# Kernel optimization log

Measured on AMD Instinct MI355X. Metric: run time of the kernel, lower is better.

## Reference

```python
import jax, jax.numpy as jnp
import numpy as np

NODE_DIM = 256
HALF = NODE_DIM // 2  # 128

# COCO-17 hierarchical grouping (from the torch module, num_joints == 17)
ORDER_1_HEAD = np.array([0, 1, 2, 3, 4])                                   # group 0: 5 joints
ORDER_1_PAIRS = np.array([(5, 6), (7, 9), (8, 10), (11, 12), (13, 15), (14, 16)])  # groups 1..6
ORDER_2_PAIRS = np.array([(0, 1), (1, 2), (1, 3), (1, 4), (4, 5), (4, 6)])


def setup_inputs() -> dict:
    key = jax.random.key(0)
    ks = jax.random.split(key, 9)
    N = 50000
    s = 0.02
    update = jax.random.normal(ks[0], (N, 17, NODE_DIM), dtype=jnp.float32)
    # first_layer[0]: Linear(node_dim*5 -> node_dim//2)
    W1_0 = jax.random.normal(ks[1], (HALF, 5 * NODE_DIM), dtype=jnp.float32) * s
    b1_0 = jax.random.normal(ks[2], (HALF,), dtype=jnp.float32) * s
    W1 = jax.random.normal(ks[3], (6, HALF, 2 * NODE_DIM), dtype=jnp.float32) * s
    b1 = jax.random.normal(ks[4], (6, HALF), dtype=jnp.float32) * s
    W2 = jax.random.normal(ks[5], (6, HALF, 2 * HALF), dtype=jnp.float32) * s
    b2 = jax.random.normal(ks[6], (6, HALF), dtype=jnp.float32) * s
    # final: Linear(6*HALF -> node_dim)
    Wf = jax.random.normal(ks[7], (NODE_DIM, 6 * HALF), dtype=jnp.float32) * s
    bf = jax.random.normal(ks[8], (NODE_DIM,), dtype=jnp.float32) * s
    return {"update": update, "W1_0": W1_0, "b1_0": b1_0, "W1": W1, "b1": b1,
            "W2": W2, "b2": b2, "Wf": Wf, "bf": bf}


def reference(update, W1_0, b1_0, W1, b1, W2, b2, Wf, bf):
    N = update.shape[0]
    # ---- first layer ----
    # group 0: joints (0..4) concatenated -> [N, 5*D]
    x0 = update[:, ORDER_1_HEAD].reshape(N, -1)
    h0 = jax.nn.relu(x0 @ W1_0.T + b1_0)                       # [N, HALF]
    # groups 1..6: pair gathers -> [N, 6, 2*D], batched small GEMM
    xp = update[:, ORDER_1_PAIRS].reshape(N, 6, -1)            # [N, 6, 2D]
    hp = jax.nn.relu(jnp.einsum('ngd,gkd->ngk', xp, W1) + b1)  # [N, 6, HALF]
    out_1 = jnp.concatenate([h0[:, None], hp], axis=1)         # [N, 7, HALF]
    # ---- second layer: pair gathers over out_1 ----
    x2 = out_1[:, ORDER_2_PAIRS].reshape(N, 6, -1)             # [N, 6, 2*HALF]
    out_2 = jax.nn.relu(jnp.einsum('ngd,gkd->ngk', x2, W2) + b2)  # [N, 6, HALF]
    # ---- final ----
    return jax.nn.relu(out_2.reshape(N, -1) @ Wf.T + bf)       # [N, NODE_DIM]
```

## Files before the change

### kernel.cpp

```cpp
#include <hip/hip_runtime.h>
#include <cstdint>

#define NODE_DIM 256
#define HALF 128
#define NJ 17

typedef __bf16 bf16x8 __attribute__((ext_vector_type(8)));
typedef float f32x4 __attribute__((ext_vector_type(4)));

__device__ __forceinline__ unsigned short f2bf(float f) {
  unsigned int u = __builtin_bit_cast(unsigned int, f);
  u = (u + 0x7FFFu + ((u >> 16) & 1u)) >> 16;
  return (unsigned short)u;
}

__device__ __forceinline__ unsigned int pack2(float lo, float hi) {
  return (unsigned int)f2bf(lo) | ((unsigned int)f2bf(hi) << 16);
}

__device__ const int d_P0[6] = {5, 7, 8, 11, 13, 14};
__device__ const int d_P1[6] = {6, 9, 10, 12, 15, 16};
__device__ const int d_Q0[6] = {0, 1, 1, 1, 4, 4};
__device__ const int d_Q1[6] = {1, 2, 3, 4, 5, 6};

__global__ __launch_bounds__(256) void kconv(
    const float* __restrict__ a, const float* __restrict__ b,
    const float* __restrict__ c, const float* __restrict__ d,
    unsigned short* __restrict__ dst) {
  const int na = 163840, nb = 393216, nc = 196608, nd = 196608;
  const int total = na + nb + nc + nd;
  int i = (blockIdx.x * 256 + threadIdx.x) * 4;
  if (i >= total) return;
  const float* src;
  int off;
  if (i < na) { src = a; off = i; }
  else if (i < na + nb) { src = b; off = i - na; }
  else if (i < na + nb + nc) { src = c; off = i - na - nb; }
  else { src = d; off = i - na - nb - nc; }
  float4 v = *(const float4*)(src + off);
  uint2 p;
  p.x = pack2(v.x, v.y);
  p.y = pack2(v.z, v.w);
  *(uint2*)(dst + i) = p;
}

__global__ __launch_bounds__(256) void k1_layer1(
    const float* __restrict__ upd,
    const unsigned short* __restrict__ w10,
    const unsigned short* __restrict__ w1,
    const float* __restrict__ b10,
    const float* __restrict__ b1,
    unsigned short* __restrict__ out1,
    int N, int ntiles) {
  __shared__ unsigned short sA[64 * 72];
  __shared__ unsigned short sW[128 * 72];

  const int tile = blockIdx.x % ntiles;
  const int g = blockIdx.x / ntiles;
  const int t = threadIdx.x;
  const int lane = t & 63;
  const int wv = t >> 6;
  const int l16 = lane & 15;
  const int quad = lane >> 4;
  const int node0 = tile * 64;

  const int K = (g == 0) ? 1280 : 512;
  const unsigned short* W = (g == 0) ? w10 : (w1 + (size_t)(g - 1) * 128 * 512);

  const int ar = t >> 2, al = t & 3;
  const int wr = t >> 1, wh = t & 1;

  f32x4 acc[8];
#pragma unroll
  for (int i = 0; i < 8; ++i) acc[i] = (f32x4){0.f, 0.f, 0.f, 0.f};

  int n = node0 + ar;
  if (n >= N) n = N - 1;

  const int nchunks = K >> 6;
  for (int kc = 0; kc < nchunks; ++kc) {
    const int kabs = kc << 6;
    int j;
    if (g == 0) j = kabs >> 8;
    else j = (kabs < 256) ? d_P0[g - 1] : d_P1[g - 1];

    const float* src = upd + ((size_t)n * NJ + j) * NODE_DIM + (kabs & 255) + al * 16;
    float4 f0 = *(const float4*)(src + 0);
    float4 f1 = *(const float4*)(src + 4);
    float4 f2 = *(const float4*)(src + 8);
    float4 f3 = *(const float4*)(src + 12);
    const uint4* wsrc = (const uint4*)(W + (size_t)wr * K + kabs + wh * 32);
    uint4 q0 = wsrc[0], q1 = wsrc[1], q2 = wsrc[2], q3 = wsrc[3];

    __syncthreads();
    uint4 pa0, pa1;
    pa0.x = pack2(f0.x, f0.y); pa0.y = pack2(f0.z, f0.w);
    pa0.z = pack2(f1.x, f1.y); pa0.w = pack2(f1.z, f1.w);
    pa1.x = pack2(f2.x, f2.y); pa1.y = pack2(f2.z, f2.w);
    pa1.z = pack2(f3.x, f3.y); pa1.w = pack2(f3.z, f3.w);
    *(uint4*)(sA + ar * 72 + al * 16) = pa0;
    *(uint4*)(sA + ar * 72 + al * 16 + 8) = pa1;
    uint4* dW = (uint4*)(sW + wr * 72 + wh * 32);
    dW[0] = q0; dW[1] = q1; dW[2] = q2; dW[3] = q3;
    __syncthreads();

#pragma unroll
    for (int kk = 0; kk < 64; kk += 32) {
      bf16x8 a = *(const bf16x8*)(sA + (wv * 16 + l16) * 72 + kk + quad * 8);
#pragma unroll
      for (int nt = 0; nt < 8; ++nt) {
        bf16x8 b = *(const bf16x8*)(sW + (nt * 16 + l16) * 72 + kk + quad * 8);
        acc[nt] = __builtin_amdgcn_mfma_f32_16x16x32_bf16(a, b, acc[nt], 0, 0, 0);
      }
    }
  }

  const float* bias = (g == 0) ? b10 : (b1 + (g - 1) * HALF);
#pragma unroll
  for (int nt = 0; nt < 8; ++nt) {
    const float bv = bias[nt * 16 + l16];
#pragma unroll
    for (int r = 0; r < 4; ++r) {
      const int node = node0 + wv * 16 + quad * 4 + r;
      if (node < N) {
        float v = acc[nt][r] + bv;
        v = v > 0.f ? v : 0.f;
        out1[(size_t)node * 896 + g * 128 + nt * 16 + l16] = f2bf(v);
      }
    }
  }
}

__global__ __launch_bounds__(256) void k2_layer2(
    const unsigned short* __restrict__ out1,
    const unsigned short* __restrict__ w2,
    const float* __restrict__ b2,
    unsigned short* __restrict__ out2,
    int N, int ntiles) {
  __shared__ unsigned short sA[64 * 72];
  __shared__ unsigned short sW[128 * 72];

  const int tile = blockIdx.x % ntiles;
  const int g = blockIdx.x / ntiles;
  const int t = threadIdx.x;
  const int lane = t & 63;
  const int wv = t >> 6;
  const int l16 = lane & 15;
  const int quad = lane >> 4;
  const int node0 = tile * 64;

  const unsigned short* W = w2 + (size_t)g * 128 * 256;
  const int ar = t >> 2, al = t & 3;
  const int wr = t >> 1, wh = t & 1;

  f32x4 acc[8];
#pragma unroll
  for (int i = 0; i < 8; ++i) acc[i] = (f32x4){0.f, 0.f, 0.f, 0.f};

  int n = node0 + ar;
  if (n >= N) n = N - 1;
  const int p0 = d_Q0[g], p1 = d_Q1[g];

  for (int kc = 0; kc < 4; ++kc) {
    const int kabs = kc << 6;
    const int grp = (kabs < 128) ? p0 : p1;
    const unsigned short* srcA = out1 + (size_t)n * 896 + grp * 128 + (kabs & 127) + al * 16;
    const uint4* asrc = (const uint4*)srcA;
    uint4 va0 = asrc[0], va1 = asrc[1];
    const uint4* wsrc = (const uint4*)(W + (size_t)wr * 256 + kabs + wh * 32);
    uint4 q0 = wsrc[0], q1 = wsrc[1], q2 = wsrc[2], q3 = wsrc[3];

    __syncthreads();
    uint4* dA = (uint4*)(sA + ar * 72 + al * 16);
    dA[0] = va0; dA[1] = va1;
    uint4* dW = (uint4*)(sW + wr * 72 + wh * 32);
    dW[0] = q0; dW[1] = q1; dW[2] = q2; dW[3] = q3;
    __syncthreads();

#pragma unroll
    for (int kk = 0; kk < 64; kk += 32) {
      bf16x8 a = *(const bf16x8*)(sA + (wv * 16 + l16) * 72 + kk + quad * 8);
#pragma unroll
      for (int nt = 0; nt < 8; ++nt) {
        bf16x8 b = *(const bf16x8*)(sW + (nt * 16 + l16) * 72 + kk + quad * 8);
        acc[nt] = __builtin_amdgcn_mfma_f32_16x16x32_bf16(a, b, acc[nt], 0, 0, 0);
      }
    }
  }

  const float* bias = b2 + g * HALF;
#pragma unroll
  for (int nt = 0; nt < 8; ++nt) {
    const float bv = bias[nt * 16 + l16];
#pragma unroll
    for (int r = 0; r < 4; ++r) {
      const int node = node0 + wv * 16 + quad * 4 + r;
      if (node < N) {
        float v = acc[nt][r] + bv;
        v = v > 0.f ? v : 0.f;
        out2[(size_t)node * 768 + g * 128 + nt * 16 + l16] = f2bf(v);
      }
    }
  }
}

__global__ __launch_bounds__(256) void k3_final(
    const unsigned short* __restrict__ out2,
    const unsigned short* __restrict__ wf,
    const float* __restrict__ bf_,
    float* __restrict__ out,
    int N) {
  __shared__ unsigned short sA[64 * 72];
  __shared__ unsigned short sW[256 * 72];

  const int t = threadIdx.x;
  const int lane = t & 63;
  const int wv = t >> 6;
  const int l16 = lane & 15;
  const int quad = lane >> 4;
  const int node0 = blockIdx.x * 64;

  const int ar = t >> 2, al = t & 3;

  f32x4 acc[16];
#pragma unroll
  for (int i = 0; i < 16; ++i) acc[i] = (f32x4){0.f, 0.f, 0.f, 0.f};

  int n = node0 + ar;
  if (n >= N) n = N - 1;

  for (int kc = 0; kc < 12; ++kc) {
    const int kabs = kc << 6;
    const uint4* asrc = (const uint4*)(out2 + (size_t)n * 768 + kabs + al * 16);
    uint4 va0 = asrc[0], va1 = asrc[1];
    const uint4* wsrc = (const uint4*)(wf + (size_t)t * 768 + kabs);
    uint4 q0 = wsrc[0], q1 = wsrc[1], q2 = wsrc[2], q3 = wsrc[3];
    uint4 q4 = wsrc[4], q5 = wsrc[5], q6 = wsrc[6], q7 = wsrc[7];

    __syncthreads();
    uint4* dA = (uint4*)(sA + ar * 72 + al * 16);
    dA[0] = va0; dA[1] = va1;
    uint4* dW = (uint4*)(sW + t * 72);
    dW[0] = q0; dW[1] = q1; dW[2] = q2; dW[3] = q3;
    dW[4] = q4; dW[5] = q5; dW[6] = q6; dW[7] = q7;
    __syncthreads();

#pragma unroll
    for (int kk = 0; kk < 64; kk += 32) {
      bf16x8 a = *(const bf16x8*)(sA + (wv * 16 + l16) * 72 + kk + quad * 8);
#pragma unroll
      for (int nt = 0; nt < 16; ++nt) {
        bf16x8 b = *(const bf16x8*)(sW + (nt * 16 + l16) * 72 + kk + quad * 8);
        acc[nt] = __builtin_amdgcn_mfma_f32_16x16x32_bf16(a, b, acc[nt], 0, 0, 0);
      }
    }
  }

#pragma unroll
  for (int nt = 0; nt < 16; ++nt) {
    const float bv = bf_[nt * 16 + l16];
#pragma unroll
    for (int r = 0; r < 4; ++r) {
      const int node = node0 + wv * 16 + quad * 4 + r;
      if (node < N) {
        float v = acc[nt][r] + bv;
        v = v > 0.f ? v : 0.f;
        out[(size_t)node * 256 + nt * 16 + l16] = v;
      }
    }
  }
}

extern "C" void kernel_launch(void* const* d_in, const int* in_sizes, int n_in,
                              void* d_out, int out_size, void* d_ws, size_t ws_size,
                              hipStream_t stream) {
  const float* upd = (const float*)d_in[0];
  const float* W10f = (const float*)d_in[1];
  const float* b10 = (const float*)d_in[2];
  const float* W1f = (const float*)d_in[3];
  const float* b1 = (const float*)d_in[4];
  const float* W2f = (const float*)d_in[5];
  const float* b2 = (const float*)d_in[6];
  const float* Wff = (const float*)d_in[7];
  const float* bff = (const float*)d_in[8];

  const int N = in_sizes[0] / (NJ * NODE_DIM);
  const int ntiles = (N + 63) / 64;

  unsigned short* wbf = (unsigned short*)d_ws;
  unsigned short* w10 = wbf;
  unsigned short* w1 = wbf + 163840;
  unsigned short* w2 = wbf + 163840 + 393216;
  unsigned short* wf = wbf + 163840 + 393216 + 196608;
  unsigned short* out1 = (unsigned short*)((char*)d_ws + (size_t)(2u << 20));
  unsigned short* out2 = out1 + (size_t)N * 896;

  kconv<<<(237568 + 255) / 256, 256, 0, stream>>>(W10f, W1f, W2f, Wff, wbf);
  k1_layer1<<<ntiles * 7, 256, 0, stream>>>(upd, w10, w1, b10, b1, out1, N, ntiles);
  k2_layer2<<<ntiles * 6, 256, 0, stream>>>(out1, w2, b2, out2, N, ntiles);
  k3_final<<<ntiles, 256, 0, stream>>>(out2, wf, bff, (float*)d_out, N);
}
```

Before: 1.338 ms.

## Double-buffer GEMM kernels with direct global-to-LDS loads and swizzled LDS

Restructures all three GEMM kernels to double-buffer the shared-memory tiles. Weight and activation tiles are loaded straight into LDS with global_load_lds into an XOR-swizzled layout, so the next K chunk streams in while the current one feeds the MFMAs. Layers 1 and 2 now loop over all groups inside one block per node tile instead of one block per (tile, group). Their outputs are staged through LDS so each node row is written with coalesced 16-byte stores. This removes a barrier per chunk and the register round trip for loads, at the cost of more LDS per block, lower occupancy, and far fewer blocks for layers 1 and 2.

```diff
diff --git a/kernel.cpp b/kernel.cpp
--- a/kernel.cpp
+++ b/kernel.cpp
@@ -16,6 +16,12 @@
 
 __device__ __forceinline__ unsigned int pack2(float lo, float hi) {
   return (unsigned int)f2bf(lo) | ((unsigned int)f2bf(hi) << 16);
+}
+
+__device__ __forceinline__ void gload16(const void* g, void* l) {
+  __builtin_amdgcn_global_load_lds(
+      (const __attribute__((address_space(1))) unsigned int*)g,
+      (__attribute__((address_space(3))) unsigned int*)l, 16, 0, 0);
 }
 
 __device__ const int d_P0[6] = {5, 7, 8, 11, 13, 14};
@@ -44,6 +50,7 @@
   *(uint2*)(dst + i) = p;
 }
 
+
 __global__ __launch_bounds__(256) void k1_layer1(
     const float* __restrict__ upd,
     const unsigned short* __restrict__ w10,
@@ -51,81 +58,121 @@
     const float* __restrict__ b10,
     const float* __restrict__ b1,
     unsigned short* __restrict__ out1,
-    int N, int ntiles) {
-  __shared__ unsigned short sA[64 * 72];
-  __shared__ unsigned short sW[128 * 72];
-
-  const int tile = blockIdx.x % ntiles;
-  const int g = blockIdx.x / ntiles;
+    int N) {
+  __shared__ unsigned short sA[2][64 * 64];
+  __shared__ unsigned short sW[2][128 * 64];
+
   const int t = threadIdx.x;
   const int lane = t & 63;
   const int wv = t >> 6;
   const int l16 = lane & 15;
   const int quad = lane >> 4;
-  const int node0 = tile * 64;
-
-  const int K = (g == 0) ? 1280 : 512;
-  const unsigned short* W = (g == 0) ? w10 : (w1 + (size_t)(g - 1) * 128 * 512);
+  const int node0 = blockIdx.x * 64;
 
   const int ar = t >> 2, al = t & 3;
-  const int wr = t >> 1, wh = t & 1;
-
-  f32x4 acc[8];
-#pragma unroll
-  for (int i = 0; i < 8; ++i) acc[i] = (f32x4){0.f, 0.f, 0.f, 0.f};
-
-  int n = node0 + ar;
-  if (n >= N) n = N - 1;
-
-  const int nchunks = K >> 6;
-  for (int kc = 0; kc < nchunks; ++kc) {
-    const int kabs = kc << 6;
-    int j;
-    if (g == 0) j = kabs >> 8;
-    else j = (kabs < 256) ? d_P0[g - 1] : d_P1[g - 1];
-
-    const float* src = upd + ((size_t)n * NJ + j) * NODE_DIM + (kabs & 255) + al * 16;
-    float4 f0 = *(const float4*)(src + 0);
-    float4 f1 = *(const float4*)(src + 4);
-    float4 f2 = *(const float4*)(src + 8);
-    float4 f3 = *(const float4*)(src + 12);
-    const uint4* wsrc = (const uint4*)(W + (size_t)wr * K + kabs + wh * 32);
-    uint4 q0 = wsrc[0], q1 = wsrc[1], q2 = wsrc[2], q3 = wsrc[3];
-
-    __syncthreads();
-    uint4 pa0, pa1;
-    pa0.x = pack2(f0.x, f0.y); pa0.y = pack2(f0.z, f0.w);
-    pa0.z = pack2(f1.x, f1.y); pa0.w = pack2(f1.z, f1.w);
-    pa1.x = pack2(f2.x, f2.y); pa1.y = pack2(f2.z, f2.w);
-    pa1.z = pack2(f3.x, f3.y); pa1.w = pack2(f3.z, f3.w);
-    *(uint4*)(sA + ar * 72 + al * 16) = pa0;
-    *(uint4*)(sA + ar * 72 + al * 16 + 8) = pa1;
-    uint4* dW = (uint4*)(sW + wr * 72 + wh * 32);
-    dW[0] = q0; dW[1] = q1; dW[2] = q2; dW[3] = q3;
-    __syncthreads();
-
-#pragma unroll
-    for (int kk = 0; kk < 64; kk += 32) {
-      bf16x8 a = *(const bf16x8*)(sA + (wv * 16 + l16) * 72 + kk + quad * 8);
-#pragma unroll
-      for (int nt = 0; nt < 8; ++nt) {
-        bf16x8 b = *(const bf16x8*)(sW + (nt * 16 + l16) * 72 + kk + quad * 8);
-        acc[nt] = __builtin_amdgcn_mfma_f32_16x16x32_bf16(a, b, acc[nt], 0, 0, 0);
-      }
-    }
-  }
-
-  const float* bias = (g == 0) ? b10 : (b1 + (g - 1) * HALF);
-#pragma unroll
-  for (int nt = 0; nt < 8; ++nt) {
-    const float bv = bias[nt * 16 + l16];
-#pragma unroll
-    for (int r = 0; r < 4; ++r) {
-      const int node = node0 + wv * 16 + quad * 4 + r;
-      if (node < N) {
+  int an = node0 + ar;
+  if (an >= N) an = N - 1;
+
+  const int lrow = lane >> 3;
+  const int sg = ((lane & 7) ^ lrow) << 3;
+
+  for (int g = 0; g < 7; ++g) {
+    const int K = (g == 0) ? 1280 : 512;
+    const unsigned short* W = (g == 0) ? w10 : (w1 + (size_t)(g - 1) * 128 * 512);
+    const int pj0 = (g == 0) ? 0 : d_P0[g - 1];
+    const int pj1 = (g == 0) ? 0 : d_P1[g - 1];
+    const int nch = K >> 6;
+
+    f32x4 acc[8];
+#pragma unroll
+    for (int i = 0; i < 8; ++i) acc[i] = (f32x4){0.f, 0.f, 0.f, 0.f};
+
+    __syncthreads();
+
+    float4 f0, f1, f2, f3;
+    {
+#pragma unroll
+      for (int i = 0; i < 4; ++i) {
+        int c = wv * 4 + i;
+        int row = c * 8 + lrow;
+        gload16(W + (size_t)row * K + sg, &sW[0][c * 512]);
+      }
+      const int j0 = (g == 0) ? 0 : pj0;
+      const float* src = upd + ((size_t)an * NJ + j0) * NODE_DIM + al * 16;
+      f0 = *(const float4*)(src);
+      f1 = *(const float4*)(src + 4);
+      f2 = *(const float4*)(src + 8);
+      f3 = *(const float4*)(src + 12);
+    }
+
+    int buf = 0;
+    for (int kc = 0; kc < nch; ++kc) {
+      {
+        uint4 pa0, pa1;
+        pa0.x = pack2(f0.x, f0.y); pa0.y = pack2(f0.z, f0.w);
+        pa0.z = pack2(f1.x, f1.y); pa0.w = pack2(f1.z, f1.w);
+        pa1.x = pack2(f2.x, f2.y); pa1.y = pack2(f2.z, f2.w);
+        pa1.z = pack2(f3.x, f3.y); pa1.w = pack2(f3.z, f3.w);
+        const int sw0 = (al * 32) ^ ((ar & 7) << 4);
+        *(uint4*)(&sA[buf][ar * 64 + (sw0 >> 1)]) = pa0;
+        *(uint4*)(&sA[buf][ar * 64 + ((sw0 ^ 16) >> 1)]) = pa1;
+      }
+      __syncthreads();
+
+      if (kc + 1 < nch) {
+        const int kabs = (kc + 1) << 6;
+#pragma unroll
+        for (int i = 0; i < 4; ++i) {
+          int c = wv * 4 + i;
+          int row = c * 8 + lrow;
+          gload16(W + (size_t)row * K + kabs + sg, &sW[buf ^ 1][c * 512]);
+        }
+        const int j = (g == 0) ? (kabs >> 8) : ((kabs < 256) ? pj0 : pj1);
+        const float* src = upd + ((size_t)an * NJ + j) * NODE_DIM + (kabs & 255) + al * 16;
+        f0 = *(const float4*)(src);
+        f1 = *(const float4*)(src + 4);
+        f2 = *(const float4*)(src + 8);
+        f3 = *(const float4*)(src + 12);
+      }
+
+#pragma unroll
+      for (int kk = 0; kk < 2; ++kk) {
+        const int k2 = kk * 64 + quad * 16;
+        const int ksw = ((k2 ^ ((l16 & 7) << 4)) >> 1);
+        const int arow = wv * 16 + l16;
+        bf16x8 a = *(const bf16x8*)(&sA[buf][arow * 64 + ksw]);
+#pragma unroll
+        for (int nt = 0; nt < 8; ++nt) {
+          const int brow = nt * 16 + l16;
+          bf16x8 b = *(const bf16x8*)(&sW[buf][brow * 64 + ksw]);
+          acc[nt] = __builtin_amdgcn_mfma_f32_16x16x32_bf16(a, b, acc[nt], 0, 0, 0);
+        }
+      }
+      buf ^= 1;
+    }
+
+    __syncthreads();
+    unsigned short* tr = &sW[0][0];
+    const float* bias = (g == 0) ? b10 : (b1 + (g - 1) * HALF);
+#pragma unroll
+    for (int nt = 0; nt < 8; ++nt) {
+      const float bv = bias[nt * 16 + l16];
+#pragma unroll
+      for (int r = 0; r < 4; ++r) {
+        const int node = wv * 16 + quad * 4 + r;
         float v = acc[nt][r] + bv;
         v = v > 0.f ? v : 0.f;
-        out1[(size_t)node * 896 + g * 128 + nt * 16 + l16] = f2bf(v);
+        tr[node * 136 + nt * 16 + l16] = f2bf(v);
+      }
+    }
+    __syncthreads();
+    {
+      const int nodeL = t >> 2, part = t & 3;
+      const int gn = node0 + nodeL;
+      if (gn < N) {
+        const uint4* s = (const uint4*)(tr + nodeL * 136 + part * 32);
+        uint4* d = (uint4*)(out1 + (size_t)gn * 896 + g * 128 + part * 32);
+        d[0] = s[0]; d[1] = s[1]; d[2] = s[2]; d[3] = s[3];
       }
     }
   }
@@ -136,69 +183,91 @@
     const unsigned short* __restrict__ w2,
     const float* __restrict__ b2,
     unsigned short* __restrict__ out2,
-    int N, int ntiles) {
-  __shared__ unsigned short sA[64 * 72];
-  __shared__ unsigned short sW[128 * 72];
-
-  const int tile = blockIdx.x % ntiles;
-  const int g = blockIdx.x / ntiles;
+    int N) {
+  __shared__ unsigned short sA[2][64 * 64];
+  __shared__ unsigned short sW[2][128 * 64];
+
   const int t = threadIdx.x;
   const int lane = t & 63;
   const int wv = t >> 6;
   const int l16 = lane & 15;
   const int quad = lane >> 4;
-  const int node0 = tile * 64;
-
-  const unsigned short* W = w2 + (size_t)g * 128 * 256;
-  const int ar = t >> 2, al = t & 3;
-  const int wr = t >> 1, wh = t & 1;
-
-  f32x4 acc[8];
-#pragma unroll
-  for (int i = 0; i < 8; ++i) acc[i] = (f32x4){0.f, 0.f, 0.f, 0.f};
-
-  int n = node0 + ar;
-  if (n >= N) n = N - 1;
-  const int p0 = d_Q0[g], p1 = d_Q1[g];
-
-  for (int kc = 0; kc < 4; ++kc) {
-    const int kabs = kc << 6;
-    const int grp = (kabs < 128) ? p0 : p1;
-    const unsigned short* srcA = out1 + (size_t)n * 896 + grp * 128 + (kabs & 127) + al * 16;
-    const uint4* asrc = (const uint4*)srcA;
-    uint4 va0 = asrc[0], va1 = asrc[1];
-    const uint4* wsrc = (const uint4*)(W + (size_t)wr * 256 + kabs + wh * 32);
-    uint4 q0 = wsrc[0], q1 = wsrc[1], q2 = wsrc[2], q3 = wsrc[3];
-
-    __syncthreads();
-    uint4* dA = (uint4*)(sA + ar * 72 + al * 16);
-    dA[0] = va0; dA[1] = va1;
-    uint4* dW = (uint4*)(sW + wr * 72 + wh * 32);
-    dW[0] = q0; dW[1] = q1; dW[2] = q2; dW[3] = q3;
-    __syncthreads();
-
-#pragma unroll
-    for (int kk = 0; kk < 64; kk += 32) {
-      bf16x8 a = *(const bf16x8*)(sA + (wv * 16 + l16) * 72 + kk + quad * 8);
-#pragma unroll
-      for (int nt = 0; nt < 8; ++nt) {
-        bf16x8 b = *(const bf16x8*)(sW + (nt * 16 + l16) * 72 + kk + quad * 8);
-        acc[nt] = __builtin_amdgcn_mfma_f32_16x16x32_bf16(a, b, acc[nt], 0, 0, 0);
-      }
-    }
-  }
-
-  const float* bias = b2 + g * HALF;
-#pragma unroll
-  for (int nt = 0; nt < 8; ++nt) {
-    const float bv = bias[nt * 16 + l16];
-#pragma unroll
-    for (int r = 0; r < 4; ++r) {
-      const int node = node0 + wv * 16 + quad * 4 + r;
-      if (node < N) {
+  const int node0 = blockIdx.x * 64;
+
+  const int lrow = lane >> 3;
+  const int sg = ((lane & 7) ^ lrow) << 3;
+
+  for (int g = 0; g < 6; ++g) {
+    const unsigned short* W = w2 + (size_t)g * 128 * 256;
+    const int p0 = d_Q0[g], p1 = d_Q1[g];
+
+    f32x4 acc[8];
+#pragma unroll
+    for (int i = 0; i < 8; ++i) acc[i] = (f32x4){0.f, 0.f, 0.f, 0.f};
+
+    auto stage = [&](int b, int kc) {
+      const int kabs = kc << 6;
+      const int grp = (kabs < 128) ? p0 : p1;
+      const int kin = kabs & 127;
+#pragma unroll
+      for (int i = 0; i < 2; ++i) {
+        int c = wv * 2 + i;
+        int row = c * 8 + lrow;
+        int gn = node0 + row; if (gn >= N) gn = N - 1;
+        gload16(out1 + (size_t)gn * 896 + grp * 128 + kin + sg, &sA[b][c * 512]);
+      }
+#pragma unroll
+      for (int i = 0; i < 4; ++i) {
+        int c = wv * 4 + i;
+        int row = c * 8 + lrow;
+        gload16(W + row * 256 + kabs + sg, &sW[b][c * 512]);
+      }
+    };
+
+    __syncthreads();
+    stage(0, 0);
+    int buf = 0;
+    for (int kc = 0; kc < 4; ++kc) {
+      __syncthreads();
+      if (kc + 1 < 4) stage(buf ^ 1, kc + 1);
+#pragma unroll
+      for (int kk = 0; kk < 2; ++kk) {
+        const int k2 = kk * 64 + quad * 16;
+        const int ksw = ((k2 ^ ((l16 & 7) << 4)) >> 1);
+        const int arow = wv * 16 + l16;
+        bf16x8 a = *(const bf16x8*)(&sA[buf][arow * 64 + ksw]);
+#pragma unroll
+        for (int nt = 0; nt < 8; ++nt) {
+          const int brow = nt * 16 + l16;
+          bf16x8 b = *(const bf16x8*)(&sW[buf][brow * 64 + ksw]);
+          acc[nt] = __builtin_amdgcn_mfma_f32_16x16x32_bf16(a, b, acc[nt], 0, 0, 0);
+        }
+      }
+      buf ^= 1;
+    }
+
+    __syncthreads();
+    unsigned short* tr = &sW[0][0];
+    const float* bias = b2 + g * HALF;
+#pragma unroll
+    for (int nt = 0; nt < 8; ++nt) {
+      const float bv = bias[nt * 16 + l16];
+#pragma unroll
+      for (int r = 0; r < 4; ++r) {
+        const int node = wv * 16 + quad * 4 + r;
         float v = acc[nt][r] + bv;
         v = v > 0.f ? v : 0.f;
-        out2[(size_t)node * 768 + g * 128 + nt * 16 + l16] = f2bf(v);
+        tr[node * 136 + nt * 16 + l16] = f2bf(v);
+      }
+    }
+    __syncthreads();
+    {
+      const int nodeL = t >> 2, part = t & 3;
+      const int gn = node0 + nodeL;
+      if (gn < N) {
+        const uint4* s = (const uint4*)(tr + nodeL * 136 + part * 32);
+        uint4* d = (uint4*)(out2 + (size_t)gn * 768 + g * 128 + part * 32);
+        d[0] = s[0]; d[1] = s[1]; d[2] = s[2]; d[3] = s[3];
       }
     }
   }
@@ -210,8 +279,8 @@
     const float* __restrict__ bf_,
     float* __restrict__ out,
     int N) {
-  __shared__ unsigned short sA[64 * 72];
-  __shared__ unsigned short sW[256 * 72];
+  __shared__ unsigned short sA[2][64 * 64];
+  __shared__ unsigned short sW[2][256 * 64];
 
   const int t = threadIdx.x;
   const int lane = t & 63;
@@ -220,40 +289,49 @@
   const int quad = lane >> 4;
   const int node0 = blockIdx.x * 64;
 
-  const int ar = t >> 2, al = t & 3;
+  const int lrow = lane >> 3;
+  const int sg = ((lane & 7) ^ lrow) << 3;
 
   f32x4 acc[16];
 #pragma unroll
   for (int i = 0; i < 16; ++i) acc[i] = (f32x4){0.f, 0.f, 0.f, 0.f};
 
-  int n = node0 + ar;
-  if (n >= N) n = N - 1;
-
+  auto stage = [&](int b, int kc) {
+    const int kabs = kc << 6;
+#pragma unroll
+    for (int i = 0; i < 2; ++i) {
+      int c = wv * 2 + i;
+      int row = c * 8 + lrow;
+      int gn = node0 + row; if (gn >= N) gn = N - 1;
+      gload16(out2 + (size_t)gn * 768 + kabs + sg, &sA[b][c * 512]);
+    }
+#pragma unroll
+    for (int i = 0; i < 8; ++i) {
+      int c = wv * 8 + i;
+      int row = c * 8 + lrow;
+      gload16(wf + (size_t)row * 768 + kabs + sg, &sW[b][c * 512]);
+    }
+  };
+
+  stage(0, 0);
+  int buf = 0;
   for (int kc = 0; kc < 12; ++kc) {
-    const int kabs = kc << 6;
-    const uint4* asrc = (const uint4*)(out2 + (size_t)n * 768 + kabs + al * 16);
-    uint4 va0 = asrc[0], va1 = asrc[1];
-    const uint4* wsrc = (const uint4*)(wf + (size_t)t * 768 + kabs);
-    uint4 q0 = wsrc[0], q1 = wsrc[1], q2 = wsrc[2], q3 = wsrc[3];
-    uint4 q4 = wsrc[4], q5 = wsrc[5], q6 = wsrc[6], q7 = wsrc[7];
-
-    __syncthreads();
-    uint4* dA = (uint4*)(sA + ar * 72 + al * 16);
-    dA[0] = va0; dA[1] = va1;
-    uint4* dW = (uint4*)(sW + t * 72);
-    dW[0] = q0; dW[1] = q1; dW[2] = q2; dW[3] = q3;
-    dW[4] = q4; dW[5] = q5; dW[6] = q6; dW[7] = q7;
-    __syncthreads();
-
-#pragma unroll
-    for (int kk = 0; kk < 64; kk += 32) {
-      bf16x8 a = *(const bf16x8*)(sA + (wv * 16 + l16) * 72 + kk + quad * 8);
+    __syncthreads();
+    if (kc + 1 < 12) stage(buf ^ 1, kc + 1);
+#pragma unroll
+    for (int kk = 0; kk < 2; ++kk) {
+      const int k2 = kk * 64 + quad * 16;
+      const int ksw = ((k2 ^ ((l16 & 7) << 4)) >> 1);
+      const int arow = wv * 16 + l16;
+      bf16x8 a = *(const bf16x8*)(&sA[buf][arow * 64 + ksw]);
 #pragma unroll
       for (int nt = 0; nt < 16; ++nt) {
-        bf16x8 b = *(const bf16x8*)(sW + (nt * 16 + l16) * 72 + kk + quad * 8);
+        const int brow = nt * 16 + l16;
+        bf16x8 b = *(const bf16x8*)(&sW[buf][brow * 64 + ksw]);
         acc[nt] = __builtin_amdgcn_mfma_f32_16x16x32_bf16(a, b, acc[nt], 0, 0, 0);
       }
     }
+    buf ^= 1;
   }
 
 #pragma unroll
@@ -296,7 +374,7 @@
   unsigned short* out2 = out1 + (size_t)N * 896;
 
   kconv<<<(237568 + 255) / 256, 256, 0, stream>>>(W10f, W1f, W2f, Wff, wbf);
-  k1_layer1<<<ntiles * 7, 256, 0, stream>>>(upd, w10, w1, b10, b1, out1, N, ntiles);
-  k2_layer2<<<ntiles * 6, 256, 0, stream>>>(out1, w2, b2, out2, N, ntiles);
+  k1_layer1<<<ntiles, 256, 0, stream>>>(upd, w10, w1, b10, b1, out1, N);
+  k2_layer2<<<ntiles, 256, 0, stream>>>(out1, w2, b2, out2, N);
   k3_final<<<ntiles, 256, 0, stream>>>(out2, wf, bff, (float*)d_out, N);
 }
```

Result: slower. 1.412 ms (+5.5%).
